# Kernel tuning notes

Measured on AMD Instinct MI355X. Metric: run time of the kernel, lower is better.

Reference implementation:

```python
import jax, jax.numpy as jnp
import numpy as np

B, S, D, H, K = 16, 2048, 1024, 16, 31  # batch, seq, d_model, n_heads, kernel_size


def setup_inputs() -> dict:
    key = jax.random.key(0)
    ks = jax.random.split(key, 6)
    sc = 1.0 / np.sqrt(D)
    return {
        "query_sequences": jax.random.normal(ks[0], (B, S, D), jnp.float32),
        "key_sequences": jax.random.normal(ks[1], (B, S, D), jnp.float32),
        "value_sequences": jax.random.normal(ks[2], (B, S, D), jnp.float32),
        "key_value_sequence_lengths": jax.random.randint(ks[3], (B,), 1, S + 1, jnp.int32),
        "W_q": jax.random.normal(ks[4], (D, H * K), jnp.float32) * sc,  # cast_queries.weight^T
        "b_q": jnp.zeros((H * K,), jnp.float32),                        # cast_queries.bias
        "conv_bias": jnp.zeros((H,), jnp.float32),
    }


def reference(query_sequences, key_sequences, value_sequences,
              key_value_sequence_lengths, W_q, b_q, conv_bias):
    b, s, d = query_sequences.shape
    h = conv_bias.shape[0]
    k = W_q.shape[1] // h
    r = d // h
    # Generate per-position, per-head depthwise filters from the queries.
    weights = (query_sequences @ W_q + b_q).reshape(b, s, h, k)  # (B,S,H,K)
    # Split key channels into heads and reduce within each head -> (B,S,H)
    ksum = key_sequences.reshape(b, s, h, r).sum(axis=-1)
    pad_l = (k - 1) // 2
    pad_r = k - 1 - pad_l
    kpad = jnp.pad(ksum, ((0, 0), (pad_l, pad_r), (0, 0)))  # (B, S+K-1, H)
    # Cross-correlation with per-position filters:
    # out[b,t,h] = sum_j weights[b,t,h,j] * kpad[b, t+j, h]
    out = jnp.zeros((b, s, h), dtype=weights.dtype)
    for j in range(k):  # fixed small kernel loop
        out = out + weights[..., j] * kpad[:, j:j + s, :]
    out = out + conv_bias  # per-head bias
    return out.transpose(0, 2, 1)  # (B, n_heads, S)
```

## Files before the change

### kernel.cpp

```cpp
#include <hip/hip_runtime.h>
#include <hip/hip_bf16.h>

#define BB 16
#define SS 2048
#define DD 1024
#define HH 16
#define KK 31
#define HK 496

typedef float f32x16 __attribute__((ext_vector_type(16)));
typedef float f32x4 __attribute__((ext_vector_type(4)));
typedef __bf16 bf16x8 __attribute__((ext_vector_type(8)));

__device__ __forceinline__ unsigned f2bf(float x) {
  unsigned u = __float_as_uint(x);
  unsigned r = u + 0x7FFFu + ((u >> 16) & 1u);
  return r >> 16;
}

__device__ __forceinline__ void gll16(const void* g, void* l) {
  __builtin_amdgcn_global_load_lds(
      (const __attribute__((address_space(1))) unsigned int*)g,
      (__attribute__((address_space(3))) unsigned int*)l, 16, 0, 0);
}

__global__ void prep_kernel(const float* __restrict__ Wq,
                            unsigned short* __restrict__ Bimg) {
  int idx = blockIdx.x * 256 + threadIdx.x;
  int e = idx & 7;
  int lane = (idx >> 3) & 63;
  int nt = (idx >> 9) & 1;
  int w = (idx >> 10) & 7;
  int slice = (idx >> 13) & 1;
  int ks = idx >> 14;
  int k = ks * 32 + slice * 16 + (lane >> 5) * 8 + e;
  int c = w * 64 + nt * 32 + (lane & 31);
  int h = c >> 5, j = c & 31;
  float v = (j < KK) ? Wq[k * HK + h * KK + j] : 0.f;
  Bimg[idx] = (unsigned short)f2bf(v);
}

__global__ __launch_bounds__(256) void ksum_kernel(const float* __restrict__ key,
                                                   float* __restrict__ ksum) {
  const int tid = threadIdx.x;
  const int r0 = blockIdx.x * 16;
#pragma unroll 4
  for (int rr = 0; rr < 16; ++rr) {
    const int row = r0 + rr;
    const f32x4 v = *((const f32x4*)(key + (size_t)row * DD) + tid);
    float p = v.x + v.y + v.z + v.w;
    p += __shfl_xor(p, 1);
    p += __shfl_xor(p, 2);
    p += __shfl_xor(p, 4);
    p += __shfl_xor(p, 8);
    if ((tid & 15) == 0) ksum[(size_t)row * HH + (tid >> 4)] = p;
  }
}

__global__ __launch_bounds__(512, 4) void mca_kernel(
    const float* __restrict__ q, const float* __restrict__ bq,
    const float* __restrict__ convb, const float* __restrict__ ksum,
    const unsigned short* __restrict__ Bimg, float* __restrict__ out) {
  extern __shared__ char smem[];
  const int tid = threadIdx.x;
  const int w = tid >> 6, lane = tid & 63;
  const int l31 = lane & 31, hi = lane >> 5;
  const int bid = blockIdx.x;
  const int bb = bid >> 5;
  const int t0 = (bid & 31) << 6;

  char* const A0 = smem;
  char* const A1 = smem + 8192;
  char* const B0 = smem + 16384;
  char* const B1 = smem + 49152;

  const float* qblk = q + ((size_t)(bb * SS + t0)) * DD;
  const char* const BimgB = (const char*)Bimg;

  const int arow = tid >> 3;
  const int ac16 = tid & 7;
  const float* aSrc = qblk + (size_t)arow * DD + ((ac16 ^ (arow & 7)) << 2);

  f32x16 acc[2][2];
#pragma unroll
  for (int mt = 0; mt < 2; ++mt)
#pragma unroll
    for (int nt = 0; nt < 2; ++nt)
#pragma unroll
      for (int r = 0; r < 16; ++r) acc[mt][nt][r] = 0.f;

  auto stage = [&](int ks, bool odd) {
    char* Ad = odd ? A1 : A0;
    char* Bd = odd ? B1 : B0;
    gll16(aSrc + ks * 32, Ad + w * 1024);
#pragma unroll
    for (int r = 0; r < 4; ++r)
      gll16(BimgB + (size_t)ks * 32768 + r * 8192 + (size_t)tid * 16,
            Bd + r * 8192 + w * 1024);
  };

  auto afrag = [&](const char* Ad, int s, int mt) -> bf16x8 {
    const int row = mt * 32 + l31;
    const int u = s * 2 + hi;
    const int g0 = (2 * u) ^ (row & 7);
    const int g1 = (2 * u + 1) ^ (row & 7);
    const f32x4 lo = *(const f32x4*)(Ad + row * 128 + g0 * 16);
    const f32x4 hh = *(const f32x4*)(Ad + row * 128 + g1 * 16);
    unsigned p0, p1, p2, p3;
    asm("v_cvt_pk_bf16_f32 %0, %1, %2" : "=v"(p0) : "v"(lo.x), "v"(lo.y));
    asm("v_cvt_pk_bf16_f32 %0, %1, %2" : "=v"(p1) : "v"(lo.z), "v"(lo.w));
    asm("v_cvt_pk_bf16_f32 %0, %1, %2" : "=v"(p2) : "v"(hh.x), "v"(hh.y));
    asm("v_cvt_pk_bf16_f32 %0, %1, %2" : "=v"(p3) : "v"(hh.z), "v"(hh.w));
    union { unsigned u4[4]; bf16x8 b; } cv;
    cv.u4[0] = p0; cv.u4[1] = p1; cv.u4[2] = p2; cv.u4[3] = p3;
    return cv.b;
  };
  auto bfrag = [&](const char* Bd, int s, int nt) -> bf16x8 {
    return *(const bf16x8*)(Bd + s * 16384 + nt * 1024 + w * 2048 + lane * 16);
  };
  auto compute = [&](const char* Ad, const char* Bd) {
#pragma unroll
    for (int s = 0; s < 2; ++s) {
      bf16x8 b0 = bfrag(Bd, s, 0);
      bf16x8 b1 = bfrag(Bd, s, 1);
      bf16x8 a0 = afrag(Ad, s, 0);
      bf16x8 a1 = afrag(Ad, s, 1);
      acc[0][0] = __builtin_amdgcn_mfma_f32_32x32x16_bf16(a0, b0, acc[0][0], 0, 0, 0);
      acc[1][0] = __builtin_amdgcn_mfma_f32_32x32x16_bf16(a1, b0, acc[1][0], 0, 0, 0);
      acc[0][1] = __builtin_amdgcn_mfma_f32_32x32x16_bf16(a0, b1, acc[0][1], 0, 0, 0);
      acc[1][1] = __builtin_amdgcn_mfma_f32_32x32x16_bf16(a1, b1, acc[1][1], 0, 0, 0);
    }
  };

  stage(0, false);
  stage(1, true);
  asm volatile("s_waitcnt vmcnt(5)" ::: "memory");
  __builtin_amdgcn_sched_barrier(0);
  __builtin_amdgcn_s_barrier();

#pragma unroll 2
  for (int ks = 0; ks < 30; ++ks) {
    const bool odd = ks & 1;
    compute(odd ? A1 : A0, odd ? B1 : B0);
    __builtin_amdgcn_s_barrier();
    __builtin_amdgcn_sched_barrier(0);
    stage(ks + 2, odd);
    asm volatile("s_waitcnt vmcnt(5)" ::: "memory");
    __builtin_amdgcn_sched_barrier(0);
    __builtin_amdgcn_s_barrier();
  }
  compute(A0, B0);
  asm volatile("s_waitcnt vmcnt(0)" ::: "memory");
  __builtin_amdgcn_sched_barrier(0);
  __builtin_amdgcn_s_barrier();
  compute(A1, B1);

  float bqv[2], cb[2];
#pragma unroll
  for (int nt = 0; nt < 2; ++nt) {
    const int h = w * 2 + nt;
    bqv[nt] = (l31 < KK) ? bq[h * KK + l31] : 0.f;
    cb[nt] = convb[h];
  }

  __syncthreads();
  float* kl = reinterpret_cast<float*>(smem);
  for (int i = tid; i < 96 * 16; i += 512) {
    int trow = i >> 4, h = i & 15;
    int t = t0 + trow - 15;
    kl[trow * 17 + h] = (t >= 0 && t < SS) ? ksum[((size_t)bb * SS + t) * HH + h] : 0.f;
  }
  __syncthreads();

#pragma unroll
  for (int mt = 0; mt < 2; ++mt)
#pragma unroll
    for (int nt = 0; nt < 2; ++nt) {
      const int h = w * 2 + nt;
#pragma unroll
      for (int r = 0; r < 16; ++r) {
        const int tl = mt * 32 + (r & 3) + 8 * (r >> 2) + 4 * hi;
        float v = (acc[mt][nt][r] + bqv[nt]) * kl[(tl + l31) * 17 + h];
        v += __shfl_xor(v, 1);
        v += __shfl_xor(v, 2);
        v += __shfl_xor(v, 4);
        v += __shfl_xor(v, 8);
        v += __shfl_xor(v, 16);
        if (l31 == r)
          out[((size_t)(bb * HH + h)) * SS + t0 + tl] = v + cb[nt];
      }
    }
}

extern "C" void kernel_launch(void* const* d_in, const int* in_sizes, int n_in,
                              void* d_out, int out_size, void* d_ws, size_t ws_size,
                              hipStream_t stream) {
  const float* q   = (const float*)d_in[0];
  const float* key = (const float*)d_in[1];
  const float* Wq  = (const float*)d_in[4];
  const float* bq  = (const float*)d_in[5];
  const float* cvb = (const float*)d_in[6];
  float* out = (float*)d_out;

  float* ksum = (float*)d_ws;
  unsigned short* Bimg = (unsigned short*)((char*)d_ws + (2 << 20));

  hipFuncSetAttribute((const void*)mca_kernel,
                      hipFuncAttributeMaxDynamicSharedMemorySize, 81920);

  prep_kernel<<<2048, 256, 0, stream>>>(Wq, Bimg);
  ksum_kernel<<<2048, 256, 0, stream>>>(key, ksum);
  mca_kernel<<<BB * (SS / 64), 512, 81920, stream>>>(q, bq, cvb, ksum, Bimg, out);
}
```

Baseline: 97.13 us.

## Double the M tile per block and switch to a three-stage LDS pipeline

Each block now computes 128 query rows instead of 64, so every block reuses each staged filter-weight tile across four MFMA row tiles, and the grid is halved. The K loop moves from double buffering to a three-buffer ring of 48KB stages with adjusted vmcnt waits, and the loop is fully unrolled. Shared memory grows to 144KB and the occupancy hint drops to 2, so each CU likely holds only one block. That trades latency hiding from concurrent blocks for deeper prefetch and less redundant B loading.

```diff
diff --git a/kernel.cpp b/kernel.cpp
--- a/kernel.cpp
+++ b/kernel.cpp
@@ -57,7 +57,7 @@
   }
 }
 
-__global__ __launch_bounds__(512, 4) void mca_kernel(
+__global__ __launch_bounds__(512, 2) void mca_kernel(
     const float* __restrict__ q, const float* __restrict__ bq,
     const float* __restrict__ convb, const float* __restrict__ ksum,
     const unsigned short* __restrict__ Bimg, float* __restrict__ out) {
@@ -66,33 +66,29 @@
   const int w = tid >> 6, lane = tid & 63;
   const int l31 = lane & 31, hi = lane >> 5;
   const int bid = blockIdx.x;
-  const int bb = bid >> 5;
-  const int t0 = (bid & 31) << 6;
-
-  char* const A0 = smem;
-  char* const A1 = smem + 8192;
-  char* const B0 = smem + 16384;
-  char* const B1 = smem + 49152;
+  const int bb = bid >> 4;
+  const int t0 = (bid & 15) << 7;
 
   const float* qblk = q + ((size_t)(bb * SS + t0)) * DD;
   const char* const BimgB = (const char*)Bimg;
 
-  const int arow = tid >> 3;
-  const int ac16 = tid & 7;
-  const float* aSrc = qblk + (size_t)arow * DD + ((ac16 ^ (arow & 7)) << 2);
-
-  f32x16 acc[2][2];
-#pragma unroll
-  for (int mt = 0; mt < 2; ++mt)
+  const int g0r = tid >> 3, gs = tid & 7;
+  const int g1r = g0r + 64;
+  const float* aS0 = qblk + (size_t)g0r * DD + ((gs ^ (g0r & 7)) << 2);
+  const float* aS1 = qblk + (size_t)g1r * DD + ((gs ^ (g1r & 7)) << 2);
+
+  f32x16 acc[4][2];
+#pragma unroll
+  for (int mt = 0; mt < 4; ++mt)
 #pragma unroll
     for (int nt = 0; nt < 2; ++nt)
 #pragma unroll
       for (int r = 0; r < 16; ++r) acc[mt][nt][r] = 0.f;
 
-  auto stage = [&](int ks, bool odd) {
-    char* Ad = odd ? A1 : A0;
-    char* Bd = odd ? B1 : B0;
-    gll16(aSrc + ks * 32, Ad + w * 1024);
+  auto stage = [&](int ks, char* base) {
+    gll16(aS0 + ks * 32, base + w * 1024);
+    gll16(aS1 + ks * 32, base + 8192 + w * 1024);
+    char* Bd = base + 16384;
 #pragma unroll
     for (int r = 0; r < 4; ++r)
       gll16(BimgB + (size_t)ks * 32768 + r * 8192 + (size_t)tid * 16,
@@ -102,10 +98,10 @@
   auto afrag = [&](const char* Ad, int s, int mt) -> bf16x8 {
     const int row = mt * 32 + l31;
     const int u = s * 2 + hi;
-    const int g0 = (2 * u) ^ (row & 7);
-    const int g1 = (2 * u + 1) ^ (row & 7);
-    const f32x4 lo = *(const f32x4*)(Ad + row * 128 + g0 * 16);
-    const f32x4 hh = *(const f32x4*)(Ad + row * 128 + g1 * 16);
+    const int q0 = (2 * u) ^ (row & 7);
+    const int q1 = (2 * u + 1) ^ (row & 7);
+    const f32x4 lo = *(const f32x4*)(Ad + row * 128 + q0 * 16);
+    const f32x4 hh = *(const f32x4*)(Ad + row * 128 + q1 * 16);
     unsigned p0, p1, p2, p3;
     asm("v_cvt_pk_bf16_f32 %0, %1, %2" : "=v"(p0) : "v"(lo.x), "v"(lo.y));
     asm("v_cvt_pk_bf16_f32 %0, %1, %2" : "=v"(p1) : "v"(lo.z), "v"(lo.w));
@@ -116,44 +112,50 @@
     return cv.b;
   };
   auto bfrag = [&](const char* Bd, int s, int nt) -> bf16x8 {
-    return *(const bf16x8*)(Bd + s * 16384 + nt * 1024 + w * 2048 + lane * 16);
-  };
-  auto compute = [&](const char* Ad, const char* Bd) {
+    return *(const bf16x8*)(Bd + s * 16384 + w * 2048 + nt * 1024 + lane * 16);
+  };
+  auto compute = [&](const char* base) {
+    const char* Ad = base;
+    const char* Bd = base + 16384;
 #pragma unroll
     for (int s = 0; s < 2; ++s) {
       bf16x8 b0 = bfrag(Bd, s, 0);
       bf16x8 b1 = bfrag(Bd, s, 1);
-      bf16x8 a0 = afrag(Ad, s, 0);
-      bf16x8 a1 = afrag(Ad, s, 1);
-      acc[0][0] = __builtin_amdgcn_mfma_f32_32x32x16_bf16(a0, b0, acc[0][0], 0, 0, 0);
-      acc[1][0] = __builtin_amdgcn_mfma_f32_32x32x16_bf16(a1, b0, acc[1][0], 0, 0, 0);
-      acc[0][1] = __builtin_amdgcn_mfma_f32_32x32x16_bf16(a0, b1, acc[0][1], 0, 0, 0);
-      acc[1][1] = __builtin_amdgcn_mfma_f32_32x32x16_bf16(a1, b1, acc[1][1], 0, 0, 0);
+#pragma unroll
+      for (int mt = 0; mt < 4; ++mt) {
+        bf16x8 a = afrag(Ad, s, mt);
+        acc[mt][0] = __builtin_amdgcn_mfma_f32_32x32x16_bf16(a, b0, acc[mt][0], 0, 0, 0);
+        acc[mt][1] = __builtin_amdgcn_mfma_f32_32x32x16_bf16(a, b1, acc[mt][1], 0, 0, 0);
+      }
     }
   };
 
-  stage(0, false);
-  stage(1, true);
-  asm volatile("s_waitcnt vmcnt(5)" ::: "memory");
+  stage(0, smem);
+  stage(1, smem + 49152);
+  stage(2, smem + 98304);
+  asm volatile("s_waitcnt vmcnt(12)" ::: "memory");
   __builtin_amdgcn_sched_barrier(0);
   __builtin_amdgcn_s_barrier();
-
-#pragma unroll 2
-  for (int ks = 0; ks < 30; ++ks) {
-    const bool odd = ks & 1;
-    compute(odd ? A1 : A0, odd ? B1 : B0);
+  __builtin_amdgcn_sched_barrier(0);
+
+#pragma unroll
+  for (int ks = 0; ks < 32; ++ks) {
+    char* base = smem + (ks % 3) * 49152;
+    compute(base);
     __builtin_amdgcn_s_barrier();
     __builtin_amdgcn_sched_barrier(0);
-    stage(ks + 2, odd);
-    asm volatile("s_waitcnt vmcnt(5)" ::: "memory");
+    if (ks + 3 < 32) stage(ks + 3, base);
+    if (ks < 29) {
+      asm volatile("s_waitcnt vmcnt(12)" ::: "memory");
+    } else if (ks == 29) {
+      asm volatile("s_waitcnt vmcnt(6)" ::: "memory");
+    } else if (ks == 30) {
+      asm volatile("s_waitcnt vmcnt(0)" ::: "memory");
+    }
     __builtin_amdgcn_sched_barrier(0);
     __builtin_amdgcn_s_barrier();
-  }
-  compute(A0, B0);
-  asm volatile("s_waitcnt vmcnt(0)" ::: "memory");
-  __builtin_amdgcn_sched_barrier(0);
-  __builtin_amdgcn_s_barrier();
-  compute(A1, B1);
+    __builtin_amdgcn_sched_barrier(0);
+  }
 
   float bqv[2], cb[2];
 #pragma unroll
@@ -165,7 +167,7 @@
 
   __syncthreads();
   float* kl = reinterpret_cast<float*>(smem);
-  for (int i = tid; i < 96 * 16; i += 512) {
+  for (int i = tid; i < 160 * 16; i += 512) {
     int trow = i >> 4, h = i & 15;
     int t = t0 + trow - 15;
     kl[trow * 17 + h] = (t >= 0 && t < SS) ? ksum[((size_t)bb * SS + t) * HH + h] : 0.f;
@@ -173,7 +175,7 @@
   __syncthreads();
 
 #pragma unroll
-  for (int mt = 0; mt < 2; ++mt)
+  for (int mt = 0; mt < 4; ++mt)
 #pragma unroll
     for (int nt = 0; nt < 2; ++nt) {
       const int h = w * 2 + nt;
@@ -206,9 +208,9 @@
   unsigned short* Bimg = (unsigned short*)((char*)d_ws + (2 << 20));
 
   hipFuncSetAttribute((const void*)mca_kernel,
-                      hipFuncAttributeMaxDynamicSharedMemorySize, 81920);
+                      hipFuncAttributeMaxDynamicSharedMemorySize, 147456);
 
   prep_kernel<<<2048, 256, 0, stream>>>(Wq, Bimg);
   ksum_kernel<<<2048, 256, 0, stream>>>(key, ksum);
-  mca_kernel<<<BB * (SS / 64), 512, 81920, stream>>>(q, bq, cvb, ksum, Bimg, out);
-}
+  mca_kernel<<<BB * (SS / 128), 512, 147456, stream>>>(q, bq, cvb, ksum, Bimg, out);
+}
```

New measurement: 97.52 us. About the same (+0.4%).
